# Kernel optimization log

Measured on AMD Instinct MI355X. Metric: run time of the kernel, lower is better.

## Reference

```python
import jax, jax.numpy as jnp
import numpy as np

EPS = 1e-5
SLOPE = 0.01  # LeakyReLU default negative_slope


def conv3(x, w):
    # x: [B,C,D,H,W], w: [O,I,3,3,3]; SubMConv3d on a dense grid == dense SAME conv, no bias
    return jax.lax.conv_general_dilated(
        x, w, window_strides=(1, 1, 1), padding='SAME',
        dimension_numbers=('NCDHW', 'OIDHW', 'NCDHW'))


def bn_c(x, g, b, m, v):
    # BatchNorm1d (eval) over channel axis 1 of [B,C,D,H,W]
    s = (1.0, -1, 1, 1, 1)
    return (x - m.reshape(1, -1, 1, 1, 1)) * (g.reshape(1, -1, 1, 1, 1) * jax.lax.rsqrt(v.reshape(1, -1, 1, 1, 1) + EPS)) + b.reshape(1, -1, 1, 1, 1)


def bn_f(x, g, b, m, v):
    # BatchNorm1d (eval) over last (feature) axis
    return (x - m) * (g * jax.lax.rsqrt(v + EPS)) + b


def lrelu(x):
    return jnp.where(x > 0, x, SLOPE * x)


def setup_inputs() -> dict:
    key = jax.random.key(0)
    ks = jax.random.split(key, 32)
    B, C, D, H, W = 2, 256, 64, 64, 16
    N = 100000
    init_size, emb = 32, 3

    fea = jax.random.normal(ks[0], (B, C, D, H, W), dtype=jnp.float32)
    gi0 = jax.random.randint(ks[1], (B, N), 0, D)
    gi1 = jax.random.randint(ks[2], (B, N), 0, H)
    gi2 = jax.random.randint(ks[3], (B, N), 0, W)
    grid_ind = jnp.stack([gi0, gi1, gi2], axis=-1).astype(jnp.int32)  # [B,N,3]
    xyz = jax.random.normal(ks[4], (B, N, 3), dtype=jnp.float32)

    def bn_params(k, c):
        k1, k2, k3, k4 = jax.random.split(k, 4)
        return (1.0 + 0.1 * jax.random.normal(k1, (c,), jnp.float32),
                0.1 * jax.random.normal(k2, (c,), jnp.float32),
                0.1 * jax.random.normal(k3, (c,), jnp.float32),
                0.5 + jax.random.uniform(k4, (c,), jnp.float32))

    W1 = jax.random.normal(ks[5], (C, C, 3, 3, 3), jnp.float32) * (1.0 / np.sqrt(27 * C))
    g1, b1, m1, v1 = bn_params(ks[6], C)
    W2 = jax.random.normal(ks[7], (2 * init_size, C, 3, 3, 3), jnp.float32) * (1.0 / np.sqrt(27 * C))
    g2, b2, m2, v2 = bn_params(ks[8], 2 * init_size)
    W3 = jax.random.normal(ks[9], (init_size, 2 * init_size, 3, 3, 3), jnp.float32) * (1.0 / np.sqrt(27 * 2 * init_size))
    g3, b3, m3, v3 = bn_params(ks[10], init_size)

    Wo1 = jax.random.normal(ks[11], (init_size + 3, init_size), jnp.float32) * (1.0 / np.sqrt(init_size + 3))
    bo1 = 0.01 * jax.random.normal(ks[12], (init_size,), jnp.float32)
    go, bo, mo, vo = bn_params(ks[13], init_size)
    Wo2 = jax.random.normal(ks[14], (init_size, emb), jnp.float32) * (1.0 / np.sqrt(init_size))
    bo2 = 0.01 * jax.random.normal(ks[15], (emb,), jnp.float32)

    return dict(fea=fea, grid_ind=grid_ind, xyz=xyz,
                W1=W1, g1=g1, b1=b1, m1=m1, v1=v1,
                W2=W2, g2=g2, b2=b2, m2=m2, v2=v2,
                W3=W3, g3=g3, b3=b3, m3=m3, v3=v3,
                Wo1=Wo1, bo1=bo1, go=go, bo=bo, mo=mo, vo=vo,
                Wo2=Wo2, bo2=bo2)


def reference(fea, grid_ind, xyz,
              W1, g1, b1, m1, v1,
              W2, g2, b2, m2, v2,
              W3, g3, b3, m3, v3,
              Wo1, bo1, go, bo, mo, vo,
              Wo2, bo2):
    # sparse conv stack (dense-grid equivalent)
    x = lrelu(bn_c(conv3(fea, W1), g1, b1, m1, v1))
    x = lrelu(bn_c(conv3(x, W2), g2, b2, m2, v2))
    x = lrelu(bn_c(conv3(x, W3), g3, b3, m3, v3))  # [B, init_size, D, H, W]

    # fea.dense().permute(0,2,3,4,1) -> [B, D, H, W, C]; per-point gather
    xg = jnp.transpose(x, (0, 2, 3, 4, 1))
    B = xg.shape[0]
    bidx = jnp.arange(B)[:, None]  # [B,1]
    pt = xg[bidx, grid_ind[:, :, 0], grid_ind[:, :, 1], grid_ind[:, :, 2]]  # [B, N, init_size]

    # concat xyz, Linear -> BN -> ReLU -> Linear
    h = jnp.concatenate([pt, xyz[:, :, :3]], axis=-1)
    h = jax.nn.relu(bn_f(h @ Wo1 + bo1, go, bo, mo, vo))
    return h @ Wo2 + bo2  # [B, N, embedding_dim]
```

## Files before the change

kernel.cpp:

```cpp
#include <hip/hip_runtime.h>
#include <stdint.h>

#define EPS 1e-5f
#define SLOPE 0.01f

typedef short bf16x8 __attribute__((ext_vector_type(8)));
typedef float f32x4 __attribute__((ext_vector_type(4)));

__device__ __forceinline__ uint16_t f2bf(float x) {
  union { float f; uint32_t u; } v; v.f = x;
  return (uint16_t)((v.u + 0x7fffu + ((v.u >> 16) & 1u)) >> 16);
}

__device__ __forceinline__ void g2lds16(const void* g, void* l) {
  __builtin_amdgcn_global_load_lds(
      (const __attribute__((address_space(1))) void*)g,
      (__attribute__((address_space(3))) void*)l, 16, 0, 0);
}

__global__ void prep_bn(const float* g1, const float* b1, const float* m1, const float* v1,
                        const float* g2, const float* b2, const float* m2, const float* v2,
                        const float* g3, const float* b3, const float* m3, const float* v3,
                        const float* go, const float* bo, const float* mo, const float* vo,
                        const float* bo1,
                        float* s1, float* be1, float* s2, float* be2,
                        float* s3, float* be3, float* so, float* beo) {
  int t = threadIdx.x;
  if (t < 256) { float s = g1[t] / sqrtf(v1[t] + EPS); s1[t] = s; be1[t] = b1[t] - m1[t] * s; }
  if (t < 64)  { float s = g2[t] / sqrtf(v2[t] + EPS); s2[t] = s; be2[t] = b2[t] - m2[t] * s; }
  if (t < 32)  { float s = g3[t] / sqrtf(v3[t] + EPS); s3[t] = s; be3[t] = b3[t] - m3[t] * s; }
  if (t < 32)  { float s = go[t] / sqrtf(vo[t] + EPS); so[t] = s; beo[t] = bo[t] + (bo1[t] - mo[t]) * s; }
}

__global__ void wtrans(const float* __restrict__ W, uint16_t* __restrict__ Wt,
                       int CO, int CI) {
  int idx = blockIdx.x * 256 + threadIdx.x;
  int total = CO * CI * 27;
  if (idx >= total) return;
  int t = idx / (CO * CI);
  int rem = idx % (CO * CI);
  int co = rem / CI, ci = rem % CI;
  Wt[idx] = f2bf(W[((size_t)co * CI + ci) * 27 + t]);
}

__global__ __launch_bounds__(256) void transpose_fea(const float* __restrict__ fea,
                                                     uint16_t* __restrict__ pad0) {
  int tid = threadIdx.x;
  int idx = blockIdx.x;
  int half = idx & 1;
  int q = (idx >> 1) & 3;
  int d = (idx >> 3) & 63;
  int b = idx >> 9;
  int s = q * 256 + tid;
  int h = s >> 4, w = s & 15;
  const float* src = fea + (size_t)(b * 256 + half * 128) * 65536 + (size_t)d * 1024 + s;
  uint16_t* dst = pad0 + ((size_t)b * 78408 +
                          (size_t)((d + 1) * 1188 + (h + 1) * 18 + (w + 1))) * 256 + half * 128;
#pragma unroll 4
  for (int c8 = 0; c8 < 16; ++c8) {
    uint16_t v[8];
#pragma unroll
    for (int j = 0; j < 8; ++j)
      v[j] = f2bf(src[(size_t)(c8 * 8 + j) * 65536]);
    *(uint4*)&dst[c8 * 8] = *(uint4*)v;
  }
}

template <int CI, int CO, int MH, int WM, int WN, bool LAST>
__global__ __launch_bounds__(256, 2) void conv_mfma(const uint16_t* __restrict__ padIn,
                                                    const uint16_t* __restrict__ Wt,
                                                    const float* __restrict__ bnS,
                                                    const float* __restrict__ bnB,
                                                    uint16_t* __restrict__ padOut,
                                                    float* __restrict__ x3out) {
  constexpr int NTILE = CO;
  constexpr int MTILE = MH * 16;
  constexpr int MPW = MTILE / WM;
  constexpr int NPW = NTILE / WN;
  constexpr int MSUB = MPW / 16;
  constexpr int NSUB = NPW / 16;
  constexpr int KC = CI / 64;
  constexpr int G = 9 * KC;
  constexpr int HB = 64 / MH;
  constexpr int HALF = MH / 8;
  constexpr int ROWSTR = 18 * CI;

  __shared__ __align__(16) uint16_t Alds[2][18 * MH * 64];
  __shared__ __align__(16) uint16_t Blds[2][NTILE * 32];

  const int tid = threadIdx.x;
  const int lane = tid & 63;
  const int wv = tid >> 6;
  const int wvm = wv / WN;
  const int wvn = wv % WN;
  const int col = lane & 15;
  const int quad = lane >> 4;

  const int mt = blockIdx.x;
  const int b = mt / (64 * HB);
  const int r = mt % (64 * HB);
  const int d = r / HB;
  const int h0 = (r % HB) * MH;

  const size_t bOffIn = (size_t)b * 78408 * CI;

  const int qB = tid & 7;
  const int rB = ((tid >> 3) << 1) + (qB >> 2);
  const int uB = (qB & 3) ^ ((tid >> 3) & 3);

  const int aslot0 = wv * 5 - (wv >= 2 ? (wv - 2) : 0);
  const int anslots = (wv < 2) ? 5 : 4;

  auto stageA = [&](int dh, int kc, int as) {
    const int kd = dh / 3, kh = dh % 3;
    const uint16_t* agBase = padIn + bOffIn +
        (size_t)((d + kd) * 1188 + (h0 + kh) * 18) * CI + kc * 64 +
        (size_t)(lane >> 3) * ROWSTR;
    for (int p = 0; p < anslots; ++p) {
      int wp = aslot0 + p;
      int gu = (lane & 7) ^ (wp & 7);
#pragma unroll
      for (int hf = 0; hf < HALF; ++hf)
        g2lds16(agBase + (size_t)(hf * 8) * ROWSTR + wp * CI + gu * 8,
                (char*)Alds[as] + wp * (MH * 128) + hf * 1024);
    }
  };

  auto stageB = [&](int dh, int kc, int kw, int ks) {
    const uint16_t* bg = Wt + (size_t)((dh * 3 + kw) * CO) * CI + kc * 64 + ks * 32 + uB * 8;
    if constexpr (CO >= 64) {
#pragma unroll
      for (int p = 0; p < CO / 64; ++p)
        g2lds16(bg + (size_t)(rB + 64 * p) * CI, (char*)Blds[ks] + p * 4096 + wv * 1024);
    } else {
      if (tid < CO * 4)
        g2lds16(bg + (size_t)rB * CI, (char*)Blds[ks] + wv * 1024);
    }
  };

  f32x4 acc[MSUB][NSUB] = {};
  int acur = 0;

  auto compute = [&](int kw, int ks) {
    bf16x8 af[MSUB], bfr[NSUB];
#pragma unroll
    for (int mi = 0; mi < MSUB; ++mi) {
      int wq = col + kw;
      int u = (ks * 4 + quad) ^ (wq & 7);
      int mhIdx = wvm * MSUB + mi;
      af[mi] = *(const bf16x8*)&Alds[acur][wq * (MH * 64) + mhIdx * 64 + u * 8];
    }
#pragma unroll
    for (int ni = 0; ni < NSUB; ++ni) {
      int rw = wvn * NPW + ni * 16 + col;
      int u = quad ^ ((rw >> 1) & 3);
      bfr[ni] = *(const bf16x8*)&Blds[ks][(rw >> 1) * 64 + (rw & 1) * 32 + u * 8];
    }
#pragma unroll
    for (int mi = 0; mi < MSUB; ++mi)
#pragma unroll
      for (int ni = 0; ni < NSUB; ++ni)
        acc[mi][ni] = __builtin_amdgcn_mfma_f32_16x16x32_bf16(af[mi], bfr[ni], acc[mi][ni], 0, 0, 0);
  };

  stageA(0, 0, 0);
  stageB(0, 0, 0, 0);
  __syncthreads();

  for (int g = 0; g < G; ++g) {
    const int dh = g / KC, kc = g % KC;
    const bool more = (g + 1 < G);
    const int dhn = (kc == KC - 1) ? dh + 1 : dh;
    const int kcn = (kc == KC - 1) ? 0 : kc + 1;
#pragma unroll
    for (int s = 0; s < 6; ++s) {
      const int kw = s >> 1, ks = s & 1;
      if (s < 5) stageB(dh, kc, (s + 1) >> 1, (s + 1) & 1);
      else if (more) stageB(dhn, kcn, 0, 0);
      if (s == 4 && more) stageA(dhn, kcn, acur ^ 1);
      compute(kw, ks);
      __syncthreads();
    }
    acur ^= 1;
  }

#pragma unroll
  for (int ni = 0; ni < NSUB; ++ni) {
    const int co = wvn * NPW + ni * 16 + col;
    const float sv = bnS[co];
    const float bv = bnB[co];
#pragma unroll
    for (int mi = 0; mi < MSUB; ++mi) {
#pragma unroll
      for (int rr = 0; rr < 4; ++rr) {
        int m = wvm * MPW + mi * 16 + quad * 4 + rr;
        float v = acc[mi][ni][rr] * sv + bv;
        v = v > 0.f ? v : SLOPE * v;
        int mh = m >> 4, w = m & 15;
        if (!LAST) {
          size_t o = ((size_t)b * 78408 +
                      (size_t)((d + 1) * 1188 + (h0 + mh + 1) * 18 + (w + 1))) * CO + co;
          padOut[o] = f2bf(v);
        } else {
          size_t o = ((size_t)b * 65536 + (size_t)((d * 64 + h0 + mh) * 16 + w)) * 32 + co;
          x3out[o] = v;
        }
      }
    }
  }
}

__global__ __launch_bounds__(256) void gather_mlp(const float* __restrict__ x3,
                                                  const int* __restrict__ gidx,
                                                  const float* __restrict__ xyz,
                                                  const float* __restrict__ Wo1,
                                                  const float* __restrict__ so,
                                                  const float* __restrict__ beo,
                                                  const float* __restrict__ Wo2,
                                                  const float* __restrict__ bo2,
                                                  float* __restrict__ out) {
  __shared__ __align__(16) float w1[35 * 32];
  __shared__ float w2[32 * 3];
  __shared__ float sS[32], sB[32], b2s[3];
  int tid = threadIdx.x;
  for (int i = tid; i < 1120; i += 256) w1[i] = Wo1[i];
  if (tid < 96) w2[tid] = Wo2[tid];
  if (tid < 32) { sS[tid] = so[tid]; sB[tid] = beo[tid]; }
  if (tid < 3) b2s[tid] = bo2[tid];
  __syncthreads();

  int idx = blockIdx.x * 256 + tid;
  if (idx >= 200000) return;
  int b = idx >= 100000 ? 1 : 0;
  int gb = idx * 3;
  int i0 = gidx[gb], i1 = gidx[gb + 1], i2 = gidx[gb + 2];
  const float* pt = x3 + ((size_t)b * 65536 + (size_t)((i0 * 64 + i1) * 16 + i2)) * 32;

  float h[35];
#pragma unroll
  for (int q = 0; q < 8; ++q) {
    float4 v = *(const float4*)(pt + q * 4);
    h[q * 4] = v.x; h[q * 4 + 1] = v.y; h[q * 4 + 2] = v.z; h[q * 4 + 3] = v.w;
  }
  h[32] = xyz[gb]; h[33] = xyz[gb + 1]; h[34] = xyz[gb + 2];

  float a[32];
#pragma unroll
  for (int j = 0; j < 32; ++j) a[j] = 0.f;
#pragma unroll
  for (int k = 0; k < 35; ++k) {
    float hk = h[k];
    const float4* wr = (const float4*)(w1 + k * 32);
#pragma unroll
    for (int q = 0; q < 8; ++q) {
      float4 wv = wr[q];
      a[q * 4 + 0] += hk * wv.x;
      a[q * 4 + 1] += hk * wv.y;
      a[q * 4 + 2] += hk * wv.z;
      a[q * 4 + 3] += hk * wv.w;
    }
  }
  float o0 = b2s[0], o1 = b2s[1], o2 = b2s[2];
#pragma unroll
  for (int j = 0; j < 32; ++j) {
    float y = a[j] * sS[j] + sB[j];
    y = y > 0.f ? y : 0.f;
    o0 += y * w2[j * 3 + 0];
    o1 += y * w2[j * 3 + 1];
    o2 += y * w2[j * 3 + 2];
  }
  out[gb] = o0; out[gb + 1] = o1; out[gb + 2] = o2;
}

extern "C" void kernel_launch(void* const* d_in, const int* in_sizes, int n_in,
                              void* d_out, int out_size, void* d_ws, size_t ws_size,
                              hipStream_t stream) {
  (void)in_sizes; (void)n_in; (void)out_size;
  if (ws_size < 165130000) return;

  const float* fea = (const float*)d_in[0];
  const int*   gidx = (const int*)d_in[1];
  const float* xyz = (const float*)d_in[2];
  const float* W1 = (const float*)d_in[3];
  const float* g1 = (const float*)d_in[4];
  const float* b1 = (const float*)d_in[5];
  const float* m1 = (const float*)d_in[6];
  const float* v1 = (const float*)d_in[7];
  const float* W2 = (const float*)d_in[8];
  const float* g2 = (const float*)d_in[9];
  const float* b2 = (const float*)d_in[10];
  const float* m2 = (const float*)d_in[11];
  const float* v2 = (const float*)d_in[12];
  const float* W3 = (const float*)d_in[13];
  const float* g3 = (const float*)d_in[14];
  const float* b3 = (const float*)d_in[15];
  const float* m3 = (const float*)d_in[16];
  const float* v3 = (const float*)d_in[17];
  const float* Wo1 = (const float*)d_in[18];
  const float* bo1 = (const float*)d_in[19];
  const float* go = (const float*)d_in[20];
  const float* bo = (const float*)d_in[21];
  const float* mo = (const float*)d_in[22];
  const float* vo = (const float*)d_in[23];
  const float* Wo2 = (const float*)d_in[24];
  const float* bo2 = (const float*)d_in[25];

  char* ws = (char*)d_ws;
  uint16_t* pad0 = (uint16_t*)(ws);
  uint16_t* pad1 = (uint16_t*)(ws + 80289792);
  uint16_t* Wt1 = (uint16_t*)(ws + 160579584);
  uint16_t* Wt2 = (uint16_t*)(ws + 164118528);
  uint16_t* Wt3 = (uint16_t*)(ws + 165003264);
  float* s1  = (float*)(ws + 165113856 + 0 * 1024);
  float* be1 = (float*)(ws + 165113856 + 1 * 1024);
  float* s2  = (float*)(ws + 165113856 + 2 * 1024);
  float* be2 = (float*)(ws + 165113856 + 3 * 1024);
  float* s3  = (float*)(ws + 165113856 + 4 * 1024);
  float* be3 = (float*)(ws + 165113856 + 5 * 1024);
  float* so  = (float*)(ws + 165113856 + 6 * 1024);
  float* beo = (float*)(ws + 165113856 + 7 * 1024);
  uint16_t* pad2 = (uint16_t*)(ws);
  float* x3 = (float*)(ws + 20072448);

  hipMemsetAsync(ws, 0, 160579584, stream);

  prep_bn<<<1, 256, 0, stream>>>(g1, b1, m1, v1, g2, b2, m2, v2, g3, b3, m3, v3,
                                 go, bo, mo, vo, bo1, s1, be1, s2, be2, s3, be3, so, beo);
  wtrans<<<6912, 256, 0, stream>>>(W1, Wt1, 256, 256);
  wtrans<<<1728, 256, 0, stream>>>(W2, Wt2, 64, 256);
  wtrans<<<216, 256, 0, stream>>>(W3, Wt3, 32, 64);
  transpose_fea<<<1024, 256, 0, stream>>>(fea, pad0);

  conv_mfma<256, 256, 8, 2, 2, false>
      <<<1024, 256, 0, stream>>>(pad0, Wt1, s1, be1, pad1, nullptr);

  hipMemsetAsync(pad2, 0, 20072448, stream);

  conv_mfma<256, 64, 16, 4, 1, false>
      <<<512, 256, 0, stream>>>(pad1, Wt2, s2, be2, pad2, nullptr);

  conv_mfma<64, 32, 16, 4, 1, true>
      <<<512, 256, 0, stream>>>(pad2, Wt3, s3, be3, nullptr, x3);

  gather_mlp<<<782, 256, 0, stream>>>(x3, gidx, xyz, Wo1, so, beo, Wo2, bo2, (float*)d_out);
}
```

Measured before the change: 1.133 ms.

## Zero only padding halos and use fine-grained vmcnt waits in conv pipeline

Replaces the full-workspace memsets with a kernel that zeroes only the halo border rows and columns of the padded activation buffers, cutting the large zero-fill traffic. In the conv main loop, the full __syncthreads is replaced by explicit s_waitcnt vmcnt counts matched to the number of outstanding async global-to-LDS loads, plus raw barriers. The MFMA block is wrapped in s_setprio so math waves get scheduling priority. The goal is to let prefetches stay in flight across barriers. The risk is that the halo of pad1 is no longer explicitly zeroed, so it relies on that memory already being zero, and wrong wait counts could cause LDS races.

```diff
diff --git a/kernel.cpp b/kernel.cpp
--- a/kernel.cpp
+++ b/kernel.cpp
@@ -16,6 +16,31 @@
   __builtin_amdgcn_global_load_lds(
       (const __attribute__((address_space(1))) void*)g,
       (__attribute__((address_space(3))) void*)l, 16, 0, 0);
+}
+
+__device__ __forceinline__ void vmwait(int n) {
+  switch (n) {
+    case 0:  asm volatile("s_waitcnt vmcnt(0)"  ::: "memory"); return;
+    case 1:  asm volatile("s_waitcnt vmcnt(1)"  ::: "memory"); return;
+    case 2:  asm volatile("s_waitcnt vmcnt(2)"  ::: "memory"); return;
+    case 3:  asm volatile("s_waitcnt vmcnt(3)"  ::: "memory"); return;
+    case 4:  asm volatile("s_waitcnt vmcnt(4)"  ::: "memory"); return;
+    case 5:  asm volatile("s_waitcnt vmcnt(5)"  ::: "memory"); return;
+    case 6:  asm volatile("s_waitcnt vmcnt(6)"  ::: "memory"); return;
+    case 7:  asm volatile("s_waitcnt vmcnt(7)"  ::: "memory"); return;
+    case 8:  asm volatile("s_waitcnt vmcnt(8)"  ::: "memory"); return;
+    case 9:  asm volatile("s_waitcnt vmcnt(9)"  ::: "memory"); return;
+    case 10: asm volatile("s_waitcnt vmcnt(10)" ::: "memory"); return;
+    case 11: asm volatile("s_waitcnt vmcnt(11)" ::: "memory"); return;
+    default: asm volatile("s_waitcnt vmcnt(12)" ::: "memory"); return;
+  }
+}
+
+__device__ __forceinline__ void bar() {
+  __builtin_amdgcn_sched_barrier(0);
+  __builtin_amdgcn_s_barrier();
+  __builtin_amdgcn_sched_barrier(0);
+  asm volatile("" ::: "memory");
 }
 
 __global__ void prep_bn(const float* g1, const float* b1, const float* m1, const float* v1,
@@ -41,6 +66,25 @@
   int rem = idx % (CO * CI);
   int co = rem / CI, ci = rem % CI;
   Wt[idx] = f2bf(W[((size_t)co * CI + ci) * 27 + t]);
+}
+
+template <int C>
+__global__ __launch_bounds__(256) void halo_zero(uint16_t* __restrict__ pad) {
+  int id = blockIdx.x;
+  int h = id % 66;
+  int d = (id / 66) % 66;
+  int b = id / (66 * 66);
+  uint16_t* row = pad + ((size_t)b * 78408 + (size_t)(d * 1188 + h * 18)) * C;
+  int tid = threadIdx.x;
+  const uint4 z = make_uint4(0, 0, 0, 0);
+  if (d == 0 || d == 65 || h == 0 || h == 65) {
+    constexpr int n4 = 18 * C / 8;
+    for (int i = tid; i < n4; i += 256) ((uint4*)row)[i] = z;
+  } else {
+    constexpr int n4 = C / 8;
+    if (tid < n4) ((uint4*)row)[tid] = z;
+    else if (tid < 2 * n4) ((uint4*)(row + 17 * C))[tid - n4] = z;
+  }
 }
 
 __global__ __launch_bounds__(256) void transpose_fea(const float* __restrict__ fea,
@@ -111,6 +155,9 @@
   const int aslot0 = wv * 5 - (wv >= 2 ? (wv - 2) : 0);
   const int anslots = (wv < 2) ? 5 : 4;
 
+  const int aInstr = anslots * HALF;
+  const int bInstr = (CO >= 64) ? (CO / 64) : ((wv * 64 < CO * 4) ? 1 : 0);
+
   auto stageA = [&](int dh, int kc, int as) {
     const int kd = dh / 3, kh = dh % 3;
     const uint16_t* agBase = padIn + bOffIn +
@@ -156,16 +203,17 @@
       int u = quad ^ ((rw >> 1) & 3);
       bfr[ni] = *(const bf16x8*)&Blds[ks][(rw >> 1) * 64 + (rw & 1) * 32 + u * 8];
     }
+    __builtin_amdgcn_s_setprio(1);
 #pragma unroll
     for (int mi = 0; mi < MSUB; ++mi)
 #pragma unroll
       for (int ni = 0; ni < NSUB; ++ni)
         acc[mi][ni] = __builtin_amdgcn_mfma_f32_16x16x32_bf16(af[mi], bfr[ni], acc[mi][ni], 0, 0, 0);
+    __builtin_amdgcn_s_setprio(0);
   };
 
   stageA(0, 0, 0);
   stageB(0, 0, 0, 0);
-  __syncthreads();
 
   for (int g = 0; g < G; ++g) {
     const int dh = g / KC, kc = g % KC;
@@ -175,11 +223,14 @@
 #pragma unroll
     for (int s = 0; s < 6; ++s) {
       const int kw = s >> 1, ks = s & 1;
-      if (s < 5) stageB(dh, kc, (s + 1) >> 1, (s + 1) & 1);
-      else if (more) stageB(dhn, kcn, 0, 0);
-      if (s == 4 && more) stageA(dhn, kcn, acur ^ 1);
+      int issued = 0;
+      if (s < 5) { stageB(dh, kc, (s + 1) >> 1, (s + 1) & 1); issued = bInstr; }
+      else if (more) { stageB(dhn, kcn, 0, 0); issued = bInstr; }
+      if (s == 4 && more) { stageA(dhn, kcn, acur ^ 1); issued += aInstr; }
+      vmwait(issued + ((s == 5 && more) ? aInstr : 0));
+      bar();
       compute(kw, ks);
-      __syncthreads();
+      bar();
     }
     acur ^= 1;
   }
@@ -322,19 +373,18 @@
   uint16_t* pad2 = (uint16_t*)(ws);
   float* x3 = (float*)(ws + 20072448);
 
-  hipMemsetAsync(ws, 0, 160579584, stream);
-
   prep_bn<<<1, 256, 0, stream>>>(g1, b1, m1, v1, g2, b2, m2, v2, g3, b3, m3, v3,
                                  go, bo, mo, vo, bo1, s1, be1, s2, be2, s3, be3, so, beo);
   wtrans<<<6912, 256, 0, stream>>>(W1, Wt1, 256, 256);
   wtrans<<<1728, 256, 0, stream>>>(W2, Wt2, 64, 256);
   wtrans<<<216, 256, 0, stream>>>(W3, Wt3, 32, 64);
+  halo_zero<256><<<17424, 256, 0, stream>>>(pad0);
   transpose_fea<<<1024, 256, 0, stream>>>(fea, pad0);
 
   conv_mfma<256, 256, 8, 2, 2, false>
       <<<1024, 256, 0, stream>>>(pad0, Wt1, s1, be1, pad1, nullptr);
 
-  hipMemsetAsync(pad2, 0, 20072448, stream);
+  halo_zero<64><<<8712, 256, 0, stream>>>(pad2);
 
   conv_mfma<256, 64, 16, 4, 1, false>
       <<<512, 256, 0, stream>>>(pad1, Wt2, s2, be2, pad2, nullptr);
```

After: 1.134 ms. Within noise of the previous version (+0.1%).
